# Kernel tuning notes

Measured on AMD Instinct MI355X. Metric: run time of the kernel, lower is better.

Reference implementation:

```python
import jax, jax.numpy as jnp
import numpy as np

N_TIME = 512          # n_time_nodes
LATENT = 32           # latent_dim
HIDDEN = 64           # hidden_dim
N_MODES = 8           # r_fourier_modes
X_A0 = 0.3            # initial stoichiometry (anode)
CSANMAX = 28700.0     # max concentration scale
BASE_LOGIT = float(np.log(X_A0 / (1.0 - X_A0)))  # logit_from_fraction(x_a0)
FEAT_DIM = 1 + 2 * N_MODES   # [rho, cos(k*pi*rho), sin(k*pi*rho)]
IN_DIM = LATENT + FEAT_DIM
N_POINTS = 2_000_000


def setup_inputs() -> dict:
    key = jax.random.key(0)
    ks = jax.random.split(key, 8)
    time_idx = jax.random.randint(ks[0], (N_POINTS,), 0, N_TIME)
    rho = jax.random.uniform(ks[1], (N_POINTS,), dtype=jnp.float32)
    # trainable latent code per nonzero time node
    emb = jax.random.normal(ks[2], (N_TIME - 1, LATENT), dtype=jnp.float32) * 0.02
    # decoder_a: Linear(IN,HID)+SiLU, Linear(HID,HID)+SiLU, Linear(HID,1)
    W0 = jax.random.normal(ks[3], (IN_DIM, HIDDEN), dtype=jnp.float32) / np.sqrt(IN_DIM)
    b0 = jnp.zeros((HIDDEN,), jnp.float32)
    W1 = jax.random.normal(ks[4], (HIDDEN, HIDDEN), dtype=jnp.float32) / np.sqrt(HIDDEN)
    b1 = jnp.zeros((HIDDEN,), jnp.float32)
    Wout = jax.random.normal(ks[5], (HIDDEN, 1), dtype=jnp.float32) * 0.1
    bout = jnp.zeros((1,), jnp.float32)
    return {"time_idx": time_idx, "rho": rho, "emb": emb,
            "W0": W0, "b0": b0, "W1": W1, "b1": b1, "Wout": Wout, "bout": bout}


def _radius_features(rho):
    # [N] -> [N, 1 + 2*N_MODES]
    k = jnp.arange(1, N_MODES + 1, dtype=rho.dtype)
    ang = jnp.pi * rho[:, None] * k[None, :]
    return jnp.concatenate([rho[:, None], jnp.cos(ang), jnp.sin(ang)], axis=1)


def reference(time_idx, rho, emb, W0, b0, W1, b1, Wout, bout):
    # predicated version of the torch masked scatter: compute everywhere,
    # select initial-condition value where time_idx == 0
    idx = jnp.clip(time_idx - 1, 0, N_TIME - 2)       # safe gather index
    e = emb[idx]                                       # [N, LATENT]
    feat = _radius_features(rho)                       # [N, FEAT_DIM]
    h = jnp.concatenate([e, feat], axis=1)             # [N, IN_DIM]
    h = jax.nn.silu(h @ W0 + b0)
    h = jax.nn.silu(h @ W1 + b1)
    raw = (h @ Wout + bout)[:, 0]                      # [N]
    theta = jax.nn.sigmoid(raw + BASE_LOGIT)
    return jnp.where(time_idx == 0, X_A0 * CSANMAX, theta * CSANMAX)
```

## Files before the change

### kernel.cpp

```cpp
#include <hip/hip_runtime.h>
#include <stdint.h>


typedef _Float16 half8  __attribute__((ext_vector_type(8)));
typedef _Float16 half4v __attribute__((ext_vector_type(4)));
typedef _Float16 half2v __attribute__((ext_vector_type(2)));
typedef float f32x4 __attribute__((ext_vector_type(4)));

#define LOG2E 1.44269504088896340736f
#define NLN2  -0.6931471805599453f
#define CSCL  -1.44269504088896340736f
#define BASE_LOGIT -0.84729786038720367f
#define CSANMAX 28700.0f
#define IC_VAL 8610.0f

__device__ __forceinline__ float fast_exp2(float x) { return __builtin_amdgcn_exp2f(x); }
__device__ __forceinline__ float fast_rcp(float x)  { return __builtin_amdgcn_rcpf(x); }
__device__ __forceinline__ float sigf(float x)  { return fast_rcp(1.0f + fast_exp2(-LOG2E * x)); }
__device__ __forceinline__ void usilu2(float u0, float u1, float& p0, float& p1) {
  const float d0 = 1.0f + fast_exp2(u0);
  const float d1 = 1.0f + fast_exp2(u1);
  const float r  = fast_rcp(d0 * d1);
  p0 = u0 * d1 * r;
  p1 = u1 * d0 * r;
}
__device__ __forceinline__ half2v pkh(float a, float b) {
  return __builtin_bit_cast(half2v, __builtin_amdgcn_cvt_pkrtz(a, b));
}

union H8 { half8 v8; half2v v2[4]; };
union H4 { half4v v4; half2v v2[2]; };

template <int CTRL>
__device__ __forceinline__ float dpp_radd(float x) {
  int yi = __builtin_amdgcn_update_dpp(0, __builtin_bit_cast(int, x), CTRL, 0xF, 0xF, false);
  return x + __builtin_bit_cast(float, yi);
}
__device__ __forceinline__ float row_sum16(float x) {
  x = dpp_radd<0xB1>(x);
  x = dpp_radd<0x4E>(x);
  x = dpp_radd<0x141>(x);
  x = dpp_radd<0x140>(x);
  return x;
}

__global__ __launch_bounds__(256, 4) void mlp_kernel(
    const int* __restrict__ tix, const float* __restrict__ rho,
    const float* __restrict__ emb, const float* __restrict__ W0,
    const float* __restrict__ b0, const float* __restrict__ W1,
    const float* __restrict__ b1, const float* __restrict__ Wout,
    const float* __restrict__ bout, float* __restrict__ out, int ntiles)
{
  __shared__ __align__(16) _Float16 Wlds0[2][4][64][8];
  __shared__ __align__(16) _Float16 Wlds1[2][4][64][8];
  __shared__ __align__(16) _Float16 ldsH[4][16][72];

  const int tid  = threadIdx.x;
  const int wid  = tid >> 6;
  const int lane = tid & 63;
  const int m    = lane & 15;
  const int q    = lane >> 4;

  _Float16 (*Hb)[72] = ldsH[wid];

  if (wid == 0) {
#pragma unroll
    for (int t = 0; t < 4; ++t) {
#pragma unroll
      for (int s = 0; s < 2; ++s) {
        half8 f0, f1;
#pragma unroll
        for (int j = 0; j < 8; ++j) {
          const int k = s * 32 + q * 8 + j;
          const int n = t * 16 + m;
          float v0;
          if (k < 32) {
            v0 = W0[k * 64 + n];
          } else {
            const int kn = k - 32;
            v0 = (kn < 16) ? W0[(33 + kn) * 64 + n]
               : (kn == 16) ? W0[32 * 64 + n]
               : (kn == 17) ? b0[n] : 0.0f;
          }
          f0[j] = (_Float16)(CSCL * v0);
          f1[j] = (_Float16)W1[k * 64 + n];
        }
        *(half8*)&Wlds0[s][t][lane][0] = f0;
        *(half8*)&Wlds1[s][t][lane][0] = f1;
      }
    }
  }

  float bvt[4];
  float woutm[4];
#pragma unroll
  for (int t = 0; t < 4; ++t) {
    bvt[t]   = CSCL * b1[t * 16 + m];
    woutm[t] = NLN2 * Wout[t * 16 + m];
  }
  const float boutBL = bout[0] + BASE_LOGIT;

  __syncthreads();

  half8 w0A[4], w0B[4], w1A[4], w1B[4];
#pragma unroll
  for (int t = 0; t < 4; ++t) {
    w0A[t] = *(const half8*)&Wlds0[0][t][lane][0];
    w0B[t] = *(const half8*)&Wlds0[1][t][lane][0];
    w1A[t] = *(const half8*)&Wlds1[0][t][lane][0];
    w1B[t] = *(const half8*)&Wlds1[1][t][lane][0];
  }

  const f32x4 z = {0.0f, 0.0f, 0.0f, 0.0f};
  const int tstride = gridDim.x * 4;

  int tg = blockIdx.x * 4 + wid;
  if (tg >= ntiles) return;

  int   tq = tix[tg * 16 + m];
  float rh = rho[tg * 16 + m];

  while (tg < ntiles) {
    const int   curT = tq;
    const float rhp  = rh;
    const int   tn   = tg + tstride;
    if (tn < ntiles) {
      tq = tix[tn * 16 + m];
      rh = rho[tn * 16 + m];
    }

    const int idxm = min(max(curT - 1, 0), 510);
    const float* erow = emb + (size_t)idxm * 32 + q * 8;
    const f32x4 e0 = *(const f32x4*)erow;
    const f32x4 e1 = *(const f32x4*)(erow + 4);

    const float rev = 0.5f * rhp;
    const float c1  = __builtin_amdgcn_cosf(rev);
    const float s1f = __builtin_amdgcn_sinf(rev);
    const float tc  = 2.0f * c1;
    const float x1v = (q == 0) ? c1 : ((q == 1) ? s1f : 0.0f);
    const float x0v = (q == 0) ? 1.0f : 0.0f;
    const float x2v = tc * x1v - x0v;
    const float x3v = tc * x2v - x1v;
    const float x4v = tc * x3v - x2v;
    const float x5v = tc * x4v - x3v;
    const float x6v = tc * x5v - x4v;
    const float x7v = tc * x6v - x5v;
    const float x8v = tc * x7v - x6v;
    H8 X1;
    X1.v2[0] = (q == 2) ? pkh(rhp, 1.0f) : pkh(x1v, x2v);
    X1.v2[1] = pkh(x3v, x4v);
    X1.v2[2] = pkh(x5v, x6v);
    X1.v2[3] = pkh(x7v, x8v);
    H8 X0;
    X0.v2[0] = pkh(e0[0], e0[1]); X0.v2[1] = pkh(e0[2], e0[3]);
    X0.v2[2] = pkh(e1[0], e1[1]); X0.v2[3] = pkh(e1[2], e1[3]);

    f32x4 acc[4];
#pragma unroll
    for (int t = 0; t < 4; ++t) {
      f32x4 a = __builtin_amdgcn_mfma_f32_16x16x32_f16(w0A[t], X0.v8, z, 0, 0, 0);
      a = __builtin_amdgcn_mfma_f32_16x16x32_f16(w0B[t], X1.v8, a, 0, 0, 0);
      acc[t] = a;
    }
#pragma unroll
    for (int t = 0; t < 4; ++t) {
      float p0, p1, p2, p3;
      usilu2(acc[t][0], acc[t][1], p0, p1);
      usilu2(acc[t][2], acc[t][3], p2, p3);
      H4 hh;
      hh.v2[0] = pkh(p0, p1);
      hh.v2[1] = pkh(p2, p3);
      *(half4v*)&Hb[m][t * 16 + q * 4] = hh.v4;
    }

    const half8 Y0 = *(const half8*)&Hb[m][q * 8];
    const half8 Y1 = *(const half8*)&Hb[m][32 + q * 8];
#pragma unroll
    for (int t = 0; t < 4; ++t) {
      f32x4 a = __builtin_amdgcn_mfma_f32_16x16x32_f16(Y0, w1A[t], z, 0, 0, 0);
      a = __builtin_amdgcn_mfma_f32_16x16x32_f16(Y1, w1B[t], a, 0, 0, 0);
      acc[t] = a;
    }
    float dot0 = 0.0f, dot1 = 0.0f, dot2 = 0.0f, dot3 = 0.0f;
#pragma unroll
    for (int t = 0; t < 4; ++t) {
      float p0, p1, p2, p3;
      usilu2(acc[t][0] + bvt[t], acc[t][1] + bvt[t], p0, p1);
      usilu2(acc[t][2] + bvt[t], acc[t][3] + bvt[t], p2, p3);
      dot0 = fmaf(p0, woutm[t], dot0);
      dot1 = fmaf(p1, woutm[t], dot1);
      dot2 = fmaf(p2, woutm[t], dot2);
      dot3 = fmaf(p3, woutm[t], dot3);
    }
    dot0 = row_sum16(dot0);
    dot1 = row_sum16(dot1);
    dot2 = row_sum16(dot2);
    dot3 = row_sum16(dot3);
    const float dsel = (m & 2) ? ((m & 1) ? dot3 : dot2) : ((m & 1) ? dot1 : dot0);
    const float dg = __shfl(dsel, (m >> 2) * 16 + (m & 3), 64);

    const float theta = sigf(dg + boutBL);
    const float val = (curT == 0) ? IC_VAL : theta * CSANMAX;
    if (q == 0) out[tg * 16 + m] = val;

    tg = tn;
  }
}

extern "C" void kernel_launch(void* const* d_in, const int* in_sizes, int n_in,
                              void* d_out, int out_size, void* d_ws, size_t ws_size,
                              hipStream_t stream) {
  const int*   tix  = (const int*)d_in[0];
  const float* rho  = (const float*)d_in[1];
  const float* emb  = (const float*)d_in[2];
  const float* W0   = (const float*)d_in[3];
  const float* b0   = (const float*)d_in[4];
  const float* W1   = (const float*)d_in[5];
  const float* b1   = (const float*)d_in[6];
  const float* Wout = (const float*)d_in[7];
  const float* bout = (const float*)d_in[8];
  float* outp = (float*)d_out;

  const int n      = in_sizes[0];
  const int ntiles = n / 16;

  int grid = 1024;
  const int maxg = (ntiles + 3) / 4;
  if (grid > maxg) grid = maxg;
  mlp_kernel<<<dim3(grid), dim3(256), 0, stream>>>(
      tix, rho, emb, W0, b0, W1, b1, Wout, bout, outp, ntiles);
}
```

Measured before the change: 167.5 us.

## Deepen index/embedding prefetch, reload W1 from LDS per tile, alias LDS

The loop now prefetches time indices and rho two tiles ahead, and gathers the embedding rows one tile ahead, so the dependent global gather latency overlaps with compute. The W1 fragments are no longer held in registers across the loop; they are re-read from LDS each iteration, with an asm barrier to stop hoisting. This frees VGPRs for occupancy at the cost of extra LDS traffic. The W0 staging buffer is unioned with the hidden-activation scratch to shrink LDS, which needs an extra barrier, and the grid is doubled to 2048 blocks.

```diff
diff --git a/kernel.cpp b/kernel.cpp
--- a/kernel.cpp
+++ b/kernel.cpp
@@ -51,9 +51,11 @@
     const float* __restrict__ b1, const float* __restrict__ Wout,
     const float* __restrict__ bout, float* __restrict__ out, int ntiles)
 {
-  __shared__ __align__(16) _Float16 Wlds0[2][4][64][8];
+  __shared__ __align__(16) union {
+    _Float16 stage0[2][4][64][8];
+    _Float16 H[4][16][72];
+  } shA;
   __shared__ __align__(16) _Float16 Wlds1[2][4][64][8];
-  __shared__ __align__(16) _Float16 ldsH[4][16][72];
 
   const int tid  = threadIdx.x;
   const int wid  = tid >> 6;
@@ -61,7 +63,7 @@
   const int m    = lane & 15;
   const int q    = lane >> 4;
 
-  _Float16 (*Hb)[72] = ldsH[wid];
+  _Float16 (*Hb)[72] = shA.H[wid];
 
   if (wid == 0) {
 #pragma unroll
@@ -85,7 +87,7 @@
           f0[j] = (_Float16)(CSCL * v0);
           f1[j] = (_Float16)W1[k * 64 + n];
         }
-        *(half8*)&Wlds0[s][t][lane][0] = f0;
+        *(half8*)&shA.stage0[s][t][lane][0] = f0;
         *(half8*)&Wlds1[s][t][lane][0] = f1;
       }
     }
@@ -102,38 +104,47 @@
 
   __syncthreads();
 
-  half8 w0A[4], w0B[4], w1A[4], w1B[4];
+  half8 w0A[4], w0B[4];
 #pragma unroll
   for (int t = 0; t < 4; ++t) {
-    w0A[t] = *(const half8*)&Wlds0[0][t][lane][0];
-    w0B[t] = *(const half8*)&Wlds0[1][t][lane][0];
-    w1A[t] = *(const half8*)&Wlds1[0][t][lane][0];
-    w1B[t] = *(const half8*)&Wlds1[1][t][lane][0];
-  }
+    w0A[t] = *(const half8*)&shA.stage0[0][t][lane][0];
+    w0B[t] = *(const half8*)&shA.stage0[1][t][lane][0];
+  }
+
+  __syncthreads();
+
+  const half8* wb1 = (const half8*)&Wlds1[0][0][0][0];
 
   const f32x4 z = {0.0f, 0.0f, 0.0f, 0.0f};
   const int tstride = gridDim.x * 4;
 
   int tg = blockIdx.x * 4 + wid;
   if (tg >= ntiles) return;
-
-  int   tq = tix[tg * 16 + m];
-  float rh = rho[tg * 16 + m];
-
-  while (tg < ntiles) {
-    const int   curT = tq;
-    const float rhp  = rh;
-    const int   tn   = tg + tstride;
-    if (tn < ntiles) {
-      tq = tix[tn * 16 + m];
-      rh = rho[tn * 16 + m];
-    }
-
-    const int idxm = min(max(curT - 1, 0), 510);
-    const float* erow = emb + (size_t)idxm * 32 + q * 8;
-    const f32x4 e0 = *(const f32x4*)erow;
-    const f32x4 e1 = *(const f32x4*)(erow + 4);
-
+  const int lim = ntiles - 1;
+
+  int   t0 = tix[tg * 16 + m];
+  float r0 = rho[tg * 16 + m];
+  const int tg1 = min(tg + tstride, lim);
+  int   t1 = tix[tg1 * 16 + m];
+  float r1 = rho[tg1 * 16 + m];
+  {
+    const int idx0 = min(max(t0 - 1, 0), 510);
+  }
+  const int idx0 = min(max(t0 - 1, 0), 510);
+  const float* er0 = emb + (size_t)idx0 * 32 + q * 8;
+  f32x4 eC0 = *(const f32x4*)er0;
+  f32x4 eC1 = *(const f32x4*)(er0 + 4);
+
+  while (true) {
+    const int tg2 = min(tg + 2 * tstride, lim);
+    const int   t2 = tix[tg2 * 16 + m];
+    const float r2 = rho[tg2 * 16 + m];
+    const int idxN = min(max(t1 - 1, 0), 510);
+    const float* ern = emb + (size_t)idxN * 32 + q * 8;
+    const f32x4 eN0 = *(const f32x4*)ern;
+    const f32x4 eN1 = *(const f32x4*)(ern + 4);
+
+    const float rhp = r0;
     const float rev = 0.5f * rhp;
     const float c1  = __builtin_amdgcn_cosf(rev);
     const float s1f = __builtin_amdgcn_sinf(rev);
@@ -153,8 +164,8 @@
     X1.v2[2] = pkh(x5v, x6v);
     X1.v2[3] = pkh(x7v, x8v);
     H8 X0;
-    X0.v2[0] = pkh(e0[0], e0[1]); X0.v2[1] = pkh(e0[2], e0[3]);
-    X0.v2[2] = pkh(e1[0], e1[1]); X0.v2[3] = pkh(e1[2], e1[3]);
+    X0.v2[0] = pkh(eC0[0], eC0[1]); X0.v2[1] = pkh(eC0[2], eC0[3]);
+    X0.v2[2] = pkh(eC1[0], eC1[1]); X0.v2[3] = pkh(eC1[2], eC1[3]);
 
     f32x4 acc[4];
 #pragma unroll
@@ -163,6 +174,16 @@
       a = __builtin_amdgcn_mfma_f32_16x16x32_f16(w0B[t], X1.v8, a, 0, 0, 0);
       acc[t] = a;
     }
+
+    int z0 = 0;
+    asm volatile("" : "+v"(z0));
+    half8 w1A[4], w1B[4];
+#pragma unroll
+    for (int t = 0; t < 4; ++t) {
+      w1A[t] = wb1[z0 + t * 64 + lane];
+      w1B[t] = wb1[z0 + (4 + t) * 64 + lane];
+    }
+
 #pragma unroll
     for (int t = 0; t < 4; ++t) {
       float p0, p1, p2, p3;
@@ -201,10 +222,15 @@
     const float dg = __shfl(dsel, (m >> 2) * 16 + (m & 3), 64);
 
     const float theta = sigf(dg + boutBL);
-    const float val = (curT == 0) ? IC_VAL : theta * CSANMAX;
+    const float val = (t0 == 0) ? IC_VAL : theta * CSANMAX;
     if (q == 0) out[tg * 16 + m] = val;
 
-    tg = tn;
+    const int tgn = tg + tstride;
+    if (tgn >= ntiles) break;
+    tg = tgn;
+    t0 = t1; r0 = r1;
+    t1 = t2; r1 = r2;
+    eC0 = eN0; eC1 = eN1;
   }
 }
 
@@ -225,7 +251,7 @@
   const int n      = in_sizes[0];
   const int ntiles = n / 16;
 
-  int grid = 1024;
+  int grid = 2048;
   const int maxg = (ntiles + 3) / 4;
   if (grid > maxg) grid = maxg;
   mlp_kernel<<<dim3(grid), dim3(256), 0, stream>>>(
```

Measured after the change: 167.6 us. About the same (+0.0%).
